# Optimization experiments

Hardware: AMD Instinct MI355X
Metric: run time of the kernel (lower is better)

## Reference

```python
import jax, jax.numpy as jnp
import numpy as np

B = 131072
OBS = 64
H = 512
LAT = 512
DPC = 32  # dim_per_component -> 16 components of size 32
LN_EPS = 1e-6  # flax nn.LayerNorm default


def _variance_scaling_uniform(key, shape, scale=1.0):
    # variance_scaling(scale, 'fan_avg', 'uniform')
    fan_in, fan_out = shape[0], shape[1]
    fan_avg = (fan_in + fan_out) / 2.0
    limit = np.sqrt(3.0 * scale / fan_avg)
    return jax.random.uniform(key, shape, jnp.float32, -limit, limit)


def setup_inputs() -> dict:
    key = jax.random.key(0)
    ks = jax.random.split(key, 8)
    inp = {
        'observations': jax.random.normal(ks[0], (B, OBS), jnp.float32),
        'goals': jax.random.normal(ks[1], (B, OBS), jnp.float32),
        'W0': _variance_scaling_uniform(ks[2], (OBS, H)),
        'b0': jnp.zeros((H,), jnp.float32),
        'ln0_s': jnp.ones((H,), jnp.float32),
        'ln0_b': jnp.zeros((H,), jnp.float32),
        'W1': _variance_scaling_uniform(ks[3], (H, H)),
        'b1': jnp.zeros((H,), jnp.float32),
        'ln1_s': jnp.ones((H,), jnp.float32),
        'ln1_b': jnp.zeros((H,), jnp.float32),
        'W2': _variance_scaling_uniform(ks[4], (H, H)),
        'b2': jnp.zeros((H,), jnp.float32),
        'ln2_s': jnp.ones((H,), jnp.float32),
        'ln2_b': jnp.zeros((H,), jnp.float32),
        'W3': _variance_scaling_uniform(ks[5], (H, LAT)),
        'b3': jnp.zeros((LAT,), jnp.float32),
        'alpha': jnp.zeros((), jnp.float32),
    }
    return inp


def _layer_norm(x, scale, bias):
    m = x.mean(axis=-1, keepdims=True)
    v = ((x - m) ** 2).mean(axis=-1, keepdims=True)
    return (x - m) / jnp.sqrt(v + LN_EPS) * scale + bias


def _phi(x, W0, b0, ln0_s, ln0_b, W1, b1, ln1_s, ln1_b, W2, b2, ln2_s, ln2_b, W3, b3):
    # LayerNormMLP with activate_final=False: gelu+LN after every layer except last
    x = _layer_norm(jax.nn.gelu(x @ W0 + b0), ln0_s, ln0_b)
    x = _layer_norm(jax.nn.gelu(x @ W1 + b1), ln1_s, ln1_b)
    x = _layer_norm(jax.nn.gelu(x @ W2 + b2), ln2_s, ln2_b)
    return x @ W3 + b3


def _iqe(phi_s, phi_g, alpha):
    # reshape [B, LAT] -> [B, n_components, DPC]
    x = phi_s.reshape(*phi_s.shape[:-1], -1, DPC)
    y = phi_g.reshape(*phi_g.shape[:-1], -1, DPC)
    valid = x < y
    xy = jnp.concatenate(jnp.broadcast_arrays(x, y), axis=-1)  # [B, C, 2*DPC]
    ixy = jnp.argsort(xy, axis=-1)
    sxy = jnp.take_along_axis(xy, ixy, axis=-1)
    neg_inc = jnp.take_along_axis(valid, ixy % DPC, axis=-1) * jnp.where(ixy < DPC, -1, 1)
    neg_inp = jnp.cumsum(neg_inc, axis=-1)
    neg_f = -1.0 * (neg_inp < 0)
    neg_incf = jnp.concatenate([neg_f[..., :1], neg_f[..., 1:] - neg_f[..., :-1]], axis=-1)
    components = (sxy * neg_incf).sum(axis=-1)  # [B, C]
    a = jax.nn.sigmoid(alpha)
    return a * components.mean(axis=-1) + (1.0 - a) * components.max(axis=-1)


def reference(observations, goals, W0, b0, ln0_s, ln0_b, W1, b1, ln1_s, ln1_b,
              W2, b2, ln2_s, ln2_b, W3, b3, alpha):
    params = (W0, b0, ln0_s, ln0_b, W1, b1, ln1_s, ln1_b, W2, b2, ln2_s, ln2_b, W3, b3)
    phi_s = _phi(observations, *params)
    phi_g = _phi(goals, *params)
    return _iqe(phi_s, phi_g, alpha)
```

## Files before the change

### kernel.cpp

```cpp
#include <hip/hip_runtime.h>
#include <hip/hip_bf16.h>
#include <hip/hip_fp16.h>

typedef unsigned short u16;
typedef unsigned int u32;
typedef __attribute__((ext_vector_type(8))) _Float16 f16x8;
typedef __attribute__((ext_vector_type(4))) float f32x4;

#define ROWS 32
#define RSTR 20
#define PSTR 520

__device__ __forceinline__ float bf2f(u16 b) {
  union { u32 u; float f; } c; c.u = ((u32)b) << 16; return c.f;
}
__device__ __forceinline__ u16 f2bf(float f) {
  union { float f; u32 u; } c; c.f = f;
  u32 r = c.u + 0x7FFFu + ((c.u >> 16) & 1u);
  return (u16)(r >> 16);
}
__device__ __forceinline__ float gelu_tanh(float x) {
  float x2 = x * x;
  float t = __builtin_fmaf(0.044715f, x2, 1.0f);
  float e = __expf(-1.5957691216057308f * (x * t));
  return x * __builtin_amdgcn_rcpf(1.f + e);
}
__device__ __forceinline__ float ldp(const void* p, int i, int f32) {
  return f32 ? ((const float*)p)[i] : bf2f(((const u16*)p)[i]);
}
__device__ __forceinline__ f32x4 load4p(const void* p, int i, int f32) {
  if (f32) return *(const f32x4*)((const float*)p + i);
  ushort4 u = *(const ushort4*)((const u16*)p + i);
  return (f32x4){bf2f(u.x), bf2f(u.y), bf2f(u.z), bf2f(u.w)};
}
__device__ __forceinline__ f16x8 load8(const void* base, long off, int f32) {
  f16x8 r;
  if (f32) {
    const float4* p = (const float4*)((const float*)base + off);
    float4 a = p[0], b = p[1];
    r[0] = (_Float16)a.x; r[1] = (_Float16)a.y; r[2] = (_Float16)a.z; r[3] = (_Float16)a.w;
    r[4] = (_Float16)b.x; r[5] = (_Float16)b.y; r[6] = (_Float16)b.z; r[7] = (_Float16)b.w;
  } else {
    const u16* p = (const u16*)base + off;
#pragma unroll
    for (int i = 0; i < 8; ++i) r[i] = (_Float16)bf2f(p[i]);
  }
  return r;
}
__device__ __forceinline__ u32 encH(u32 h) {
  return (h & 0x8000u) ? (h ^ 0xFFFFu) : (h | 0x8000u);
}
__device__ __forceinline__ float decE(u32 e) {
  u32 h = (e & 0x8000u) ? (e & 0x7FFFu) : (~e & 0xFFFFu);
  return __half2float(__ushort_as_half((u16)h));
}
__device__ __forceinline__ u32 umin32(u32 a, u32 b) { return a < b ? a : b; }
__device__ __forceinline__ u32 umax32(u32 a, u32 b) { return a > b ? a : b; }
template <int CTRL>
__device__ __forceinline__ u32 dppx(u32 x) {
  return (u32)__builtin_amdgcn_mov_dpp((int)x, CTRL, 0xF, 0xF, false);
}
__device__ __forceinline__ u32 lxor(u32 x, int j) {
  if (j == 1) return dppx<0xB1>(x);
  if (j == 2) return dppx<0x4E>(x);
  if (j == 8) return dppx<0x128>(x);
  return (u32)__shfl_xor((int)x, j, 64);
}
__device__ __forceinline__ float lxorf(float x, int j) {
  if (j == 1) return __uint_as_float(dppx<0xB1>(__float_as_uint(x)));
  if (j == 2) return __uint_as_float(dppx<0x4E>(__float_as_uint(x)));
  if (j == 8) return __uint_as_float(dppx<0x128>(__float_as_uint(x)));
  return __shfl_xor(x, j, 64);
}

__global__ void detect_dtype(const u16* __restrict__ obs, int* flag) {
  int l = threadIdx.x;
  float v = fabsf(bf2f(obs[2 * l]));
  if (v != v) v = 1e30f;
#pragma unroll
  for (int m = 1; m <= 32; m <<= 1) v = fmaxf(v, __shfl_xor(v, m, 64));
  if (l == 0) *flag = (v > 1000.0f) ? 1 : 0;
}

__global__ void pack_frag(const void* __restrict__ src, u16* __restrict__ dst,
                          const int* __restrict__ flag, int total,
                          int fshift, int cishift, int tmask) {
  int id = blockIdx.x * 256 + threadIdx.x;
  if (id >= total) return;
  int j = id & 7;
  int lane = (id >> 3) & 63;
  int fi = id >> 9;
  int w = fi >> fshift;
  int rem = fi & ((1 << fshift) - 1);
  int ci = rem >> cishift;
  int t = rem & tmask;
  int q = lane >> 4, r = lane & 15;
  int ch = w * 64 + ci * 16 + r;
  int k = t * 32 + q * 8 + j;
  float v = ldp(src, k * 512 + ch, *flag);
  dst[id] = __half_as_ushort(__float2half(v));
}

__global__ __launch_bounds__(512, 4) void gciqe_main(
    const void* __restrict__ obs, const void* __restrict__ goals,
    const u16* __restrict__ wT0, const u16* __restrict__ wT1,
    const u16* __restrict__ wT2, const u16* __restrict__ wT3,
    const void* __restrict__ b0, const void* __restrict__ b1,
    const void* __restrict__ b2, const void* __restrict__ b3,
    const void* __restrict__ ls0, const void* __restrict__ lb0,
    const void* __restrict__ ls1, const void* __restrict__ lb1,
    const void* __restrict__ ls2, const void* __restrict__ lb2,
    const void* __restrict__ alphap, void* __restrict__ out,
    const int* __restrict__ flagp)
{
  __shared__ __align__(16) u16 slab[ROWS * 512];
  __shared__ __align__(16) u16 phi[ROWS * PSTR];
  __shared__ __align__(16) float red[ROWS * RSTR];

  const int f32 = *flagp;
  const int tid = threadIdx.x;
  const int lane = tid & 63, w = tid >> 6;
  const int r = lane & 15, q = lane >> 4;
  const int i0 = blockIdx.x * 16;

  f32x4 acc[4][2];

#pragma unroll
  for (int ci = 0; ci < 4; ++ci) {
    acc[ci][0] = (f32x4){0.f, 0.f, 0.f, 0.f};
    acc[ci][1] = (f32x4){0.f, 0.f, 0.f, 0.f};
  }
  {
    f16x8 bf0[2][2];
#pragma unroll
    for (int nt = 0; nt < 2; ++nt) {
      int row = nt * 16 + r;
      const void* base = (row & 1) ? goals : obs;
      long ro = (long)(i0 + (row >> 1)) * 64;
#pragma unroll
      for (int u = 0; u < 2; ++u)
        bf0[nt][u] = load8(base, ro + u * 32 + q * 8, f32);
    }
    const u16* w0base = wT0 + w * 4096;
#pragma unroll
    for (int ci = 0; ci < 4; ++ci) {
#pragma unroll
      for (int u = 0; u < 2; ++u) {
        f16x8 af = *(const f16x8*)(w0base + (ci * 2 + u) * 512 + lane * 8);
        acc[ci][0] = __builtin_amdgcn_mfma_f32_16x16x32_f16(af, bf0[0][u], acc[ci][0], 0, 0, 0);
        acc[ci][1] = __builtin_amdgcn_mfma_f32_16x16x32_f16(af, bf0[1][u], acc[ci][1], 0, 0, 0);
      }
    }
  }

  for (int l = 0; l <= 3; ++l) {
    if (l > 0) {
      const u16* wp = (l == 1) ? wT1 : (l == 2) ? wT2 : wT3;
      const u16* wbase = wp + w * 32768;
#pragma unroll
      for (int ci = 0; ci < 4; ++ci) {
        acc[ci][0] = (f32x4){0.f, 0.f, 0.f, 0.f};
        acc[ci][1] = (f32x4){0.f, 0.f, 0.f, 0.f};
      }
      f16x8 A[3][4];
#pragma unroll
      for (int u = 0; u < 4; ++u) {
        A[0][u] = *(const f16x8*)(wbase + u * 512 + lane * 8);
        A[1][u] = *(const f16x8*)(wbase + (16 + u) * 512 + lane * 8);
      }
#pragma unroll
      for (int kq = 0; kq < 4; ++kq) {
        f16x8 bfr[2][4];
#pragma unroll
        for (int nt = 0; nt < 2; ++nt)
#pragma unroll
          for (int u = 0; u < 4; ++u)
            bfr[nt][u] = *(const f16x8*)(slab + (nt * 16 + kq * 4 + u) * 512 + lane * 8);
#pragma unroll
        for (int ci = 0; ci < 4; ++ci) {
          const int s = kq * 4 + ci;
          if (s + 2 < 16) {
            const int s2 = s + 2;
            const int nci = s2 & 3, nkq = s2 >> 2;
#pragma unroll
            for (int u = 0; u < 4; ++u)
              A[s2 % 3][u] = *(const f16x8*)(wbase + (nci * 16 + nkq * 4 + u) * 512 + lane * 8);
          }
#pragma unroll
          for (int u = 0; u < 4; ++u) {
            acc[ci][0] = __builtin_amdgcn_mfma_f32_16x16x32_f16(A[s % 3][u], bfr[0][u], acc[ci][0], 0, 0, 0);
            acc[ci][1] = __builtin_amdgcn_mfma_f32_16x16x32_f16(A[s % 3][u], bfr[1][u], acc[ci][1], 0, 0, 0);
          }
        }
      }
    }

    if (l < 3) {
      const void* pb  = (l == 0) ? b0 : (l == 1) ? b1 : b2;
      const void* psl = (l == 0) ? ls0 : (l == 1) ? ls1 : ls2;
      const void* plb = (l == 0) ? lb0 : (l == 1) ? lb1 : lb2;
      float s[2] = {0.f, 0.f}, t[2] = {0.f, 0.f};
#pragma unroll
      for (int ci = 0; ci < 4; ++ci) {
        int cb = w * 64 + ci * 16 + q * 4;
        f32x4 bb = load4p(pb, cb, f32);
#pragma unroll
        for (int nt = 0; nt < 2; ++nt) {
          f32x4 v = acc[ci][nt];
          v.x = gelu_tanh(v.x + bb.x); v.y = gelu_tanh(v.y + bb.y);
          v.z = gelu_tanh(v.z + bb.z); v.w = gelu_tanh(v.w + bb.w);
          acc[ci][nt] = v;
          s[nt] += v.x + v.y + v.z + v.w;
          t[nt] += v.x * v.x + v.y * v.y + v.z * v.z + v.w * v.w;
        }
      }
#pragma unroll
      for (int nt = 0; nt < 2; ++nt) {
        s[nt] += __shfl_xor(s[nt], 16, 64); t[nt] += __shfl_xor(t[nt], 16, 64);
        s[nt] += __shfl_xor(s[nt], 32, 64); t[nt] += __shfl_xor(t[nt], 32, 64);
      }
      if (q == 0) {
        *(float2*)(red + (0 * 16 + r) * RSTR + w * 2) = make_float2(s[0], t[0]);
        *(float2*)(red + (1 * 16 + r) * RSTR + w * 2) = make_float2(s[1], t[1]);
      }
      __syncthreads();
      float mean[2], rstd[2];
#pragma unroll
      for (int nt = 0; nt < 2; ++nt) {
        int row = nt * 16 + r;
        float ts = 0.f, tq = 0.f;
#pragma unroll
        for (int p = 0; p < 4; ++p) {
          f32x4 a = *(const f32x4*)(red + row * RSTR + p * 4);
          ts += a.x + a.z; tq += a.y + a.w;
        }
        mean[nt] = ts * (1.f / 512.f);
        rstd[nt] = rsqrtf(tq * (1.f / 512.f) - mean[nt] * mean[nt] + 1e-6f);
      }
#pragma unroll
      for (int ci = 0; ci < 4; ++ci) {
        int cb = w * 64 + ci * 16 + q * 4;
        f32x4 gg = load4p(psl, cb, f32);
        f32x4 hh = load4p(plb, cb, f32);
        int fk = ((cb >> 7) << 2) + ((cb >> 5) & 3);
        int sub = (((cb >> 3) & 3) * 16 + r) * 8 + (cb & 7);
#pragma unroll
        for (int nt = 0; nt < 2; ++nt) {
          f32x4 v = acc[ci][nt];
          ushort4 o;
          o.x = __half_as_ushort(__float2half((v.x - mean[nt]) * rstd[nt] * gg.x + hh.x));
          o.y = __half_as_ushort(__float2half((v.y - mean[nt]) * rstd[nt] * gg.y + hh.y));
          o.z = __half_as_ushort(__float2half((v.z - mean[nt]) * rstd[nt] * gg.z + hh.z));
          o.w = __half_as_ushort(__float2half((v.w - mean[nt]) * rstd[nt] * gg.w + hh.w));
          *(ushort4*)(slab + (nt * 16 + fk) * 512 + sub) = o;
        }
      }
      __syncthreads();
    } else {
      __syncthreads();
#pragma unroll
      for (int ci = 0; ci < 4; ++ci) {
        int cb = w * 64 + ci * 16 + q * 4;
        f32x4 bb = load4p(b3, cb, f32);
#pragma unroll
        for (int nt = 0; nt < 2; ++nt) {
          int row = nt * 16 + r;
          f32x4 v = acc[ci][nt];
          ushort4 o;
          o.x = __half_as_ushort(__float2half(v.x + bb.x));
          o.y = __half_as_ushort(__float2half(v.y + bb.y));
          o.z = __half_as_ushort(__float2half(v.z + bb.z));
          o.w = __half_as_ushort(__float2half(v.w + bb.w));
          *(ushort4*)(phi + row * PSTR + cb) = o;
        }
      }
      __syncthreads();
    }
  }

  {
    const float al = ldp(alphap, 0, f32);
    const float aa = 1.f / (1.f + __expf(-al));
    const int h = lane >> 5, il = lane & 31;
#pragma unroll
    for (int pv = 0; pv < 2; ++pv) {
      int pL = 2 * w + pv;
      float cs = 0.f, cm = 0.f;
#pragma unroll
      for (int itb = 0; itb < 8; itb += 4) {
        u32 sv[4];
#pragma unroll
        for (int u = 0; u < 4; ++u) {
          int c = 2 * (itb + u) + h;
          u32 xh = phi[(2 * pL) * PSTR + c * 32 + il];
          u32 yh = phi[(2 * pL + 1) * PSTR + c * 32 + il];
          u32 ex = encH(xh), ey = encH(yh);
          sv[u] = (ex << 16) | ((ex < ey) ? ey : 0x03FFu);
        }
#pragma unroll
        for (int k = 2; k <= 32; k <<= 1) {
#pragma unroll
          for (int j = k >> 1; j >= 1; j >>= 1) {
            const bool up = ((il & k) == 0) == ((il & j) == 0);
#pragma unroll
            for (int u = 0; u < 4; ++u) {
              u32 so = lxor(sv[u], j);
              u32 mn = umin32(sv[u], so), mx = umax32(sv[u], so);
              sv[u] = up ? mn : mx;
            }
          }
        }
        u32 ye[4], p[4];
#pragma unroll
        for (int u = 0; u < 4; ++u) {
          ye[u] = sv[u] & 0xFFFFu;
          p[u] = __shfl_up(ye[u], 1, 32);
          if (il == 0) p[u] = 0u;
        }
#pragma unroll
        for (int d = 1; d <= 16; d <<= 1) {
#pragma unroll
          for (int u = 0; u < 4; ++u) {
            u32 t2 = __shfl_up(p[u], d, 32);
            if (il >= d) p[u] = umax32(p[u], t2);
          }
        }
        float contrib[4];
#pragma unroll
        for (int u = 0; u < 4; ++u)
          contrib[u] = fmaxf(0.f, decE(ye[u]) - decE(umax32(sv[u] >> 16, p[u])));
#pragma unroll
        for (int msk = 1; msk <= 16; msk <<= 1)
#pragma unroll
          for (int u = 0; u < 4; ++u)
            contrib[u] += lxorf(contrib[u], msk);
#pragma unroll
        for (int u = 0; u < 4; ++u) {
          cs += contrib[u];
          cm = fmaxf(cm, contrib[u]);
        }
      }
      cs += __shfl_xor(cs, 32, 64);
      cm = fmaxf(cm, __shfl_xor(cm, 32, 64));
      if (lane == 0) {
        float res = aa * (cs * (1.f / 16.f)) + (1.f - aa) * cm;
        if (f32) ((float*)out)[i0 + pL] = res;
        else ((u16*)out)[i0 + pL] = f2bf(res);
      }
    }
  }
}

extern "C" void kernel_launch(void* const* d_in, const int* in_sizes, int n_in,
                              void* d_out, int out_size, void* d_ws, size_t ws_size,
                              hipStream_t stream) {
  (void)in_sizes; (void)n_in; (void)out_size; (void)ws_size;
  const void* obs   = d_in[0];
  const void* goals = d_in[1];
  const void* W0 = d_in[2];
  const void* b0 = d_in[3];
  const void* ls0 = d_in[4];
  const void* lb0 = d_in[5];
  const void* W1 = d_in[6];
  const void* b1 = d_in[7];
  const void* ls1 = d_in[8];
  const void* lb1 = d_in[9];
  const void* W2 = d_in[10];
  const void* b2 = d_in[11];
  const void* ls2 = d_in[12];
  const void* lb2 = d_in[13];
  const void* W3 = d_in[14];
  const void* b3 = d_in[15];
  const void* alpha = d_in[16];

  int* flag = (int*)d_ws;
  u16* wT0 = (u16*)((char*)d_ws + 64);
  u16* wT1 = wT0 + 512 * 64;
  u16* wT2 = wT1 + 512 * 512;
  u16* wT3 = wT2 + 512 * 512;

  detect_dtype<<<1, 64, 0, stream>>>((const u16*)obs, flag);
  pack_frag<<<128, 256, 0, stream>>>(W0, wT0, flag, 512 * 64, 3, 1, 1);
  pack_frag<<<1024, 256, 0, stream>>>(W1, wT1, flag, 512 * 512, 6, 4, 15);
  pack_frag<<<1024, 256, 0, stream>>>(W2, wT2, flag, 512 * 512, 6, 4, 15);
  pack_frag<<<1024, 256, 0, stream>>>(W3, wT3, flag, 512 * 512, 6, 4, 15);
  gciqe_main<<<8192, 512, 0, stream>>>(obs, goals, wT0, wT1, wT2, wT3,
      b0, b1, b2, b3, ls0, lb0, ls1, lb1, ls2, lb2, alpha, d_out, flag);
}
```

Baseline: 921.0 us.

## Fold LayerNorm affine into next-layer weights and defer normalization past the GEMM

LayerNorm scale is folded into the packed weights of the next layer, and the LN bias plus layer bias are precomputed into per-channel correction vectors by a new setup kernel. The main kernel writes un-normalized GELU outputs straight to LDS and applies mean and rstd after the following matmul as a rank-1 correction, which removes one full pass and one barrier per layer. LDS slab and reduction buffers are double-buffered so the write-back can overlap reads, and the separate phi buffer is dropped in favour of reading the final slab layout directly. The A-fragment prefetch depth drops from three buffers to two. Feeding raw GELU values into fp16 and applying the correction afterward may change numerical error slightly.

```diff
diff --git a/kernel.cpp b/kernel.cpp
--- a/kernel.cpp
+++ b/kernel.cpp
@@ -9,7 +9,7 @@
 
 #define ROWS 32
 #define RSTR 20
-#define PSTR 520
+#define SLABH 16384
 
 __device__ __forceinline__ float bf2f(u16 b) {
   union { u32 u; float f; } c; c.u = ((u32)b) << 16; return c.f;
@@ -73,18 +73,46 @@
   return __shfl_xor(x, j, 64);
 }
 
-__global__ void detect_dtype(const u16* __restrict__ obs, int* flag) {
+__global__ void detect_dtype(const u16* __restrict__ obs, int* flag, float* ce) {
   int l = threadIdx.x;
   float v = fabsf(bf2f(obs[2 * l]));
   if (v != v) v = 1e30f;
 #pragma unroll
   for (int m = 1; m <= 32; m <<= 1) v = fmaxf(v, __shfl_xor(v, m, 64));
   if (l == 0) *flag = (v > 1000.0f) ? 1 : 0;
+  for (int i = l; i < 3072; i += 64) ce[i] = 0.f;
+}
+
+__global__ void compute_ce(const void* __restrict__ W1, const void* __restrict__ W2,
+                           const void* __restrict__ W3,
+                           const void* __restrict__ g0, const void* __restrict__ g1,
+                           const void* __restrict__ g2,
+                           const void* __restrict__ h0, const void* __restrict__ h1,
+                           const void* __restrict__ h2,
+                           const void* __restrict__ p1, const void* __restrict__ p2,
+                           const void* __restrict__ p3,
+                           float* __restrict__ ce, const int* __restrict__ flag) {
+  int b = blockIdx.x, l = b >> 3, kc = b & 7, ch = threadIdx.x;
+  const void* W = (l == 0) ? W1 : (l == 1) ? W2 : W3;
+  const void* g = (l == 0) ? g0 : (l == 1) ? g1 : g2;
+  const void* hb = (l == 0) ? h0 : (l == 1) ? h1 : h2;
+  const void* pb = (l == 0) ? p1 : (l == 1) ? p2 : p3;
+  const int f32 = *flag;
+  float c = 0.f, e = 0.f;
+  for (int k = kc * 64; k < kc * 64 + 64; ++k) {
+    float wv = ldp(W, k * 512 + ch, f32);
+    c = __builtin_fmaf(wv, ldp(g, k, f32), c);
+    e = __builtin_fmaf(wv, ldp(hb, k, f32), e);
+  }
+  if (kc == 0) e += ldp(pb, ch, f32);
+  atomicAdd(&ce[l * 1024 + ch], c);
+  atomicAdd(&ce[l * 1024 + 512 + ch], e);
 }
 
 __global__ void pack_frag(const void* __restrict__ src, u16* __restrict__ dst,
                           const int* __restrict__ flag, int total,
-                          int fshift, int cishift, int tmask) {
+                          int fshift, int cishift, int tmask,
+                          const void* __restrict__ gscale) {
   int id = blockIdx.x * 256 + threadIdx.x;
   if (id >= total) return;
   int j = id & 7;
@@ -98,6 +126,7 @@
   int ch = w * 64 + ci * 16 + r;
   int k = t * 32 + q * 8 + j;
   float v = ldp(src, k * 512 + ch, *flag);
+  if (gscale) v *= ldp(gscale, k, *flag);
   dst[id] = __half_as_ushort(__float2half(v));
 }
 
@@ -105,17 +134,12 @@
     const void* __restrict__ obs, const void* __restrict__ goals,
     const u16* __restrict__ wT0, const u16* __restrict__ wT1,
     const u16* __restrict__ wT2, const u16* __restrict__ wT3,
-    const void* __restrict__ b0, const void* __restrict__ b1,
-    const void* __restrict__ b2, const void* __restrict__ b3,
-    const void* __restrict__ ls0, const void* __restrict__ lb0,
-    const void* __restrict__ ls1, const void* __restrict__ lb1,
-    const void* __restrict__ ls2, const void* __restrict__ lb2,
+    const void* __restrict__ b0, const float* __restrict__ ce,
     const void* __restrict__ alphap, void* __restrict__ out,
     const int* __restrict__ flagp)
 {
-  __shared__ __align__(16) u16 slab[ROWS * 512];
-  __shared__ __align__(16) u16 phi[ROWS * PSTR];
-  __shared__ __align__(16) float red[ROWS * RSTR];
+  __shared__ __align__(16) u16 slab[2 * SLABH];
+  __shared__ __align__(16) float red[2 * ROWS * RSTR];
 
   const int f32 = *flagp;
   const int tid = threadIdx.x;
@@ -157,17 +181,16 @@
     if (l > 0) {
       const u16* wp = (l == 1) ? wT1 : (l == 2) ? wT2 : wT3;
       const u16* wbase = wp + w * 32768;
+      const u16* sb = slab + (l & 1) * SLABH;
 #pragma unroll
       for (int ci = 0; ci < 4; ++ci) {
         acc[ci][0] = (f32x4){0.f, 0.f, 0.f, 0.f};
         acc[ci][1] = (f32x4){0.f, 0.f, 0.f, 0.f};
       }
-      f16x8 A[3][4];
-#pragma unroll
-      for (int u = 0; u < 4; ++u) {
+      f16x8 A[2][4];
+#pragma unroll
+      for (int u = 0; u < 4; ++u)
         A[0][u] = *(const f16x8*)(wbase + u * 512 + lane * 8);
-        A[1][u] = *(const f16x8*)(wbase + (16 + u) * 512 + lane * 8);
-      }
 #pragma unroll
       for (int kq = 0; kq < 4; ++kq) {
         f16x8 bfr[2][4];
@@ -175,43 +198,84 @@
         for (int nt = 0; nt < 2; ++nt)
 #pragma unroll
           for (int u = 0; u < 4; ++u)
-            bfr[nt][u] = *(const f16x8*)(slab + (nt * 16 + kq * 4 + u) * 512 + lane * 8);
+            bfr[nt][u] = *(const f16x8*)(sb + (nt * 16 + kq * 4 + u) * 512 + lane * 8);
 #pragma unroll
         for (int ci = 0; ci < 4; ++ci) {
-          const int s = kq * 4 + ci;
-          if (s + 2 < 16) {
-            const int s2 = s + 2;
-            const int nci = s2 & 3, nkq = s2 >> 2;
+          const int step = kq * 4 + ci;
+          const int cur = step & 1;
+          if (step < 15) {
+            const int nstep = step + 1;
+            const int nci = nstep & 3, nkq = nstep >> 2;
 #pragma unroll
             for (int u = 0; u < 4; ++u)
-              A[s2 % 3][u] = *(const f16x8*)(wbase + (nci * 16 + nkq * 4 + u) * 512 + lane * 8);
+              A[cur ^ 1][u] = *(const f16x8*)(wbase + (nci * 16 + nkq * 4 + u) * 512 + lane * 8);
           }
 #pragma unroll
           for (int u = 0; u < 4; ++u) {
-            acc[ci][0] = __builtin_amdgcn_mfma_f32_16x16x32_f16(A[s % 3][u], bfr[0][u], acc[ci][0], 0, 0, 0);
-            acc[ci][1] = __builtin_amdgcn_mfma_f32_16x16x32_f16(A[s % 3][u], bfr[1][u], acc[ci][1], 0, 0, 0);
+            acc[ci][0] = __builtin_amdgcn_mfma_f32_16x16x32_f16(A[cur][u], bfr[0][u], acc[ci][0], 0, 0, 0);
+            acc[ci][1] = __builtin_amdgcn_mfma_f32_16x16x32_f16(A[cur][u], bfr[1][u], acc[ci][1], 0, 0, 0);
           }
         }
       }
     }
 
+    float mean[2], rstd[2], mr[2];
+    if (l > 0) {
+      const float* rb = red + (l & 1) * (ROWS * RSTR);
+#pragma unroll
+      for (int nt = 0; nt < 2; ++nt) {
+        int row = nt * 16 + r;
+        float ts = 0.f, tq = 0.f;
+#pragma unroll
+        for (int p = 0; p < 4; ++p) {
+          f32x4 a = *(const f32x4*)(rb + row * RSTR + p * 4);
+          ts += a.x + a.z; tq += a.y + a.w;
+        }
+        mean[nt] = ts * (1.f / 512.f);
+        rstd[nt] = rsqrtf(tq * (1.f / 512.f) - mean[nt] * mean[nt] + 1e-6f);
+        mr[nt] = mean[nt] * rstd[nt];
+      }
+    }
+    const float* cl = (l > 0) ? (ce + (l - 1) * 1024) : (const float*)0;
+    u16* wbp = slab + ((l + 1) & 1) * SLABH;
+
     if (l < 3) {
-      const void* pb  = (l == 0) ? b0 : (l == 1) ? b1 : b2;
-      const void* psl = (l == 0) ? ls0 : (l == 1) ? ls1 : ls2;
-      const void* plb = (l == 0) ? lb0 : (l == 1) ? lb1 : lb2;
       float s[2] = {0.f, 0.f}, t[2] = {0.f, 0.f};
 #pragma unroll
       for (int ci = 0; ci < 4; ++ci) {
         int cb = w * 64 + ci * 16 + q * 4;
-        f32x4 bb = load4p(pb, cb, f32);
+        f32x4 bb, cc, ee;
+        if (l == 0) {
+          bb = load4p(b0, cb, f32);
+        } else {
+          cc = *(const f32x4*)(cl + cb);
+          ee = *(const f32x4*)(cl + 512 + cb);
+        }
+        int fk = ((cb >> 7) << 2) + ((cb >> 5) & 3);
+        int sub = (((cb >> 3) & 3) * 16 + r) * 8 + (cb & 7);
 #pragma unroll
         for (int nt = 0; nt < 2; ++nt) {
-          f32x4 v = acc[ci][nt];
-          v.x = gelu_tanh(v.x + bb.x); v.y = gelu_tanh(v.y + bb.y);
-          v.z = gelu_tanh(v.z + bb.z); v.w = gelu_tanh(v.w + bb.w);
-          acc[ci][nt] = v;
+          f32x4 a = acc[ci][nt], pre;
+          if (l == 0) {
+            pre.x = a.x + bb.x; pre.y = a.y + bb.y;
+            pre.z = a.z + bb.z; pre.w = a.w + bb.w;
+          } else {
+            pre.x = __builtin_fmaf(a.x, rstd[nt], __builtin_fmaf(-mr[nt], cc.x, ee.x));
+            pre.y = __builtin_fmaf(a.y, rstd[nt], __builtin_fmaf(-mr[nt], cc.y, ee.y));
+            pre.z = __builtin_fmaf(a.z, rstd[nt], __builtin_fmaf(-mr[nt], cc.z, ee.z));
+            pre.w = __builtin_fmaf(a.w, rstd[nt], __builtin_fmaf(-mr[nt], cc.w, ee.w));
+          }
+          f32x4 v;
+          v.x = gelu_tanh(pre.x); v.y = gelu_tanh(pre.y);
+          v.z = gelu_tanh(pre.z); v.w = gelu_tanh(pre.w);
           s[nt] += v.x + v.y + v.z + v.w;
           t[nt] += v.x * v.x + v.y * v.y + v.z * v.z + v.w * v.w;
+          ushort4 o;
+          o.x = __half_as_ushort(__float2half(v.x));
+          o.y = __half_as_ushort(__float2half(v.y));
+          o.z = __half_as_ushort(__float2half(v.z));
+          o.w = __half_as_ushort(__float2half(v.w));
+          *(ushort4*)(wbp + (nt * 16 + fk) * 512 + sub) = o;
         }
       }
 #pragma unroll
@@ -220,58 +284,28 @@
         s[nt] += __shfl_xor(s[nt], 32, 64); t[nt] += __shfl_xor(t[nt], 32, 64);
       }
       if (q == 0) {
-        *(float2*)(red + (0 * 16 + r) * RSTR + w * 2) = make_float2(s[0], t[0]);
-        *(float2*)(red + (1 * 16 + r) * RSTR + w * 2) = make_float2(s[1], t[1]);
+        float* wrb = red + (((l + 1) & 1)) * (ROWS * RSTR);
+        *(float2*)(wrb + (0 * 16 + r) * RSTR + w * 2) = make_float2(s[0], t[0]);
+        *(float2*)(wrb + (1 * 16 + r) * RSTR + w * 2) = make_float2(s[1], t[1]);
       }
       __syncthreads();
-      float mean[2], rstd[2];
-#pragma unroll
-      for (int nt = 0; nt < 2; ++nt) {
-        int row = nt * 16 + r;
-        float ts = 0.f, tq = 0.f;
-#pragma unroll
-        for (int p = 0; p < 4; ++p) {
-          f32x4 a = *(const f32x4*)(red + row * RSTR + p * 4);
-          ts += a.x + a.z; tq += a.y + a.w;
-        }
-        mean[nt] = ts * (1.f / 512.f);
-        rstd[nt] = rsqrtf(tq * (1.f / 512.f) - mean[nt] * mean[nt] + 1e-6f);
-      }
+    } else {
 #pragma unroll
       for (int ci = 0; ci < 4; ++ci) {
         int cb = w * 64 + ci * 16 + q * 4;
-        f32x4 gg = load4p(psl, cb, f32);
-        f32x4 hh = load4p(plb, cb, f32);
+        f32x4 cc = *(const f32x4*)(cl + cb);
+        f32x4 ee = *(const f32x4*)(cl + 512 + cb);
         int fk = ((cb >> 7) << 2) + ((cb >> 5) & 3);
         int sub = (((cb >> 3) & 3) * 16 + r) * 8 + (cb & 7);
 #pragma unroll
         for (int nt = 0; nt < 2; ++nt) {
-          f32x4 v = acc[ci][nt];
+          f32x4 a = acc[ci][nt];
           ushort4 o;
-          o.x = __half_as_ushort(__float2half((v.x - mean[nt]) * rstd[nt] * gg.x + hh.x));
-          o.y = __half_as_ushort(__float2half((v.y - mean[nt]) * rstd[nt] * gg.y + hh.y));
-          o.z = __half_as_ushort(__float2half((v.z - mean[nt]) * rstd[nt] * gg.z + hh.z));
-          o.w = __half_as_ushort(__float2half((v.w - mean[nt]) * rstd[nt] * gg.w + hh.w));
-          *(ushort4*)(slab + (nt * 16 + fk) * 512 + sub) = o;
-        }
-      }
-      __syncthreads();
-    } else {
-      __syncthreads();
-#pragma unroll
-      for (int ci = 0; ci < 4; ++ci) {
-        int cb = w * 64 + ci * 16 + q * 4;
-        f32x4 bb = load4p(b3, cb, f32);
-#pragma unroll
-        for (int nt = 0; nt < 2; ++nt) {
-          int row = nt * 16 + r;
-          f32x4 v = acc[ci][nt];
-          ushort4 o;
-          o.x = __half_as_ushort(__float2half(v.x + bb.x));
-          o.y = __half_as_ushort(__float2half(v.y + bb.y));
-          o.z = __half_as_ushort(__float2half(v.z + bb.z));
-          o.w = __half_as_ushort(__float2half(v.w + bb.w));
-          *(ushort4*)(phi + row * PSTR + cb) = o;
+          o.x = __half_as_ushort(__float2half(__builtin_fmaf(a.x, rstd[nt], __builtin_fmaf(-mr[nt], cc.x, ee.x))));
+          o.y = __half_as_ushort(__float2half(__builtin_fmaf(a.y, rstd[nt], __builtin_fmaf(-mr[nt], cc.y, ee.y))));
+          o.z = __half_as_ushort(__float2half(__builtin_fmaf(a.z, rstd[nt], __builtin_fmaf(-mr[nt], cc.z, ee.z))));
+          o.w = __half_as_ushort(__float2half(__builtin_fmaf(a.w, rstd[nt], __builtin_fmaf(-mr[nt], cc.w, ee.w))));
+          *(ushort4*)(wbp + (nt * 16 + fk) * 512 + sub) = o;
         }
       }
       __syncthreads();
@@ -285,6 +319,8 @@
 #pragma unroll
     for (int pv = 0; pv < 2; ++pv) {
       int pL = 2 * w + pv;
+      const int nt3 = pL >> 3;
+      const int rr8 = ((2 * pL) & 15) * 8;
       float cs = 0.f, cm = 0.f;
 #pragma unroll
       for (int itb = 0; itb < 8; itb += 4) {
@@ -292,8 +328,9 @@
 #pragma unroll
         for (int u = 0; u < 4; ++u) {
           int c = 2 * (itb + u) + h;
-          u32 xh = phi[(2 * pL) * PSTR + c * 32 + il];
-          u32 yh = phi[(2 * pL + 1) * PSTR + c * 32 + il];
+          int ba = (nt3 * 16 + (c >> 2) * 4 + (c & 3)) * 512 + (il >> 3) * 128 + rr8 + (il & 7);
+          u32 xh = slab[ba];
+          u32 yh = slab[ba + 8];
           u32 ex = encH(xh), ey = encH(yh);
           sv[u] = (ex << 16) | ((ex < ey) ? ey : 0x03FFu);
         }
@@ -378,12 +415,15 @@
   u16* wT1 = wT0 + 512 * 64;
   u16* wT2 = wT1 + 512 * 512;
   u16* wT3 = wT2 + 512 * 512;
-
-  detect_dtype<<<1, 64, 0, stream>>>((const u16*)obs, flag);
-  pack_frag<<<128, 256, 0, stream>>>(W0, wT0, flag, 512 * 64, 3, 1, 1);
-  pack_frag<<<1024, 256, 0, stream>>>(W1, wT1, flag, 512 * 512, 6, 4, 15);
-  pack_frag<<<1024, 256, 0, stream>>>(W2, wT2, flag, 512 * 512, 6, 4, 15);
-  pack_frag<<<1024, 256, 0, stream>>>(W3, wT3, flag, 512 * 512, 6, 4, 15);
+  float* ce = (float*)((char*)d_ws + 64 + 2 * (512 * 64 + 3 * 512 * 512));
+
+  detect_dtype<<<1, 64, 0, stream>>>((const u16*)obs, flag, ce);
+  compute_ce<<<24, 512, 0, stream>>>(W1, W2, W3, ls0, ls1, ls2,
+                                     lb0, lb1, lb2, b1, b2, b3, ce, flag);
+  pack_frag<<<128, 256, 0, stream>>>(W0, wT0, flag, 512 * 64, 3, 1, 1, nullptr);
+  pack_frag<<<1024, 256, 0, stream>>>(W1, wT1, flag, 512 * 512, 6, 4, 15, ls0);
+  pack_frag<<<1024, 256, 0, stream>>>(W2, wT2, flag, 512 * 512, 6, 4, 15, ls1);
+  pack_frag<<<1024, 256, 0, stream>>>(W3, wT3, flag, 512 * 512, 6, 4, 15, ls2);
   gciqe_main<<<8192, 512, 0, stream>>>(obs, goals, wT0, wT1, wT2, wT3,
-      b0, b1, b2, b3, ls0, lb0, ls1, lb1, ls2, lb2, alpha, d_out, flag);
-}
+      b0, ce, alpha, d_out, flag);
+}
```

New measurement: 966.4 us. 4.9% more time.
